# Optimization experiments

Hardware: AMD Instinct MI355X
Metric: run time of the kernel (lower is better)

Reference implementation:

```python
import math
import jax, jax.numpy as jnp
import numpy as np

B, T, E, H = 4, 2048, 1024, 16
D = E // H          # head_dim = 64
F = D // 2          # num_pairs = 32
FREQ_SIGMA = 1.0


def _build_spiral_frequencies(num_heads, num_pairs, freq_sigma):
    indices = np.arange(num_pairs, dtype=np.float32) + 0.5
    magnitudes = np.linspace(freq_sigma / max(num_pairs, 1), freq_sigma, num_pairs, dtype=np.float32)
    head_phases = np.linspace(0.0, 2.0 * math.pi, num_heads + 1, dtype=np.float32)[:-1][:, None]
    golden = (1.0 + math.sqrt(5.0)) / 2.0
    y = np.clip(1.0 - 2.0 * indices / float(num_pairs), -1.0, 1.0)
    radius = np.sqrt(np.clip(1.0 - y ** 2, 0.0, None))
    theta = (2.0 * math.pi * indices / golden)[None, :] + head_phases
    x = radius[None, :] * np.cos(theta)
    z = radius[None, :] * np.sin(theta)
    directions = np.stack([x, np.broadcast_to(y[None, :], (num_heads, num_pairs)), z], axis=-1)
    return (directions * magnitudes[None, :, None]).astype(np.float32)  # (H, F, 3)


def setup_inputs() -> dict:
    key = jax.random.key(0)
    ks = jax.random.split(key, 4)
    query = jax.random.normal(ks[0], (B, T, E), dtype=jnp.float32)
    positions = jax.random.normal(ks[1], (B, T, 3), dtype=jnp.float32)
    in_proj_weight = jax.random.normal(ks[2], (3 * E, E), dtype=jnp.float32) * (1.0 / math.sqrt(E))
    in_proj_bias = jnp.zeros((3 * E,), dtype=jnp.float32)
    out_proj_weight = jax.random.normal(ks[3], (E, E), dtype=jnp.float32) * (1.0 / math.sqrt(E))
    out_proj_bias = jnp.zeros((E,), dtype=jnp.float32)
    freqs = jnp.asarray(_build_spiral_frequencies(H, F, FREQ_SIGMA))
    return dict(query=query, positions=positions, in_proj_weight=in_proj_weight,
                in_proj_bias=in_proj_bias, out_proj_weight=out_proj_weight,
                out_proj_bias=out_proj_bias, freqs=freqs)


def _apply_rotary(x, positions, freqs):
    # x: (B, H, T, D), positions: (B, T, 3), freqs: (H, F, 3)
    angles = jnp.einsum('btd,hfd->bhtf', positions.astype(jnp.float32), freqs.astype(jnp.float32))
    cos = jnp.cos(angles).astype(x.dtype)
    sin = jnp.sin(angles).astype(x.dtype)
    xr = x.reshape(*x.shape[:-1], F, 2)
    x0, x1 = xr[..., 0], xr[..., 1]
    rotated = jnp.stack((x0 * cos - x1 * sin, x0 * sin + x1 * cos), axis=-1)
    return rotated.reshape(x.shape)  # rotary_dim == head_dim here


def reference(query, positions, in_proj_weight, in_proj_bias, out_proj_weight, out_proj_bias, freqs):
    b, t, e = query.shape
    h = freqs.shape[0]
    d = e // h
    # QKV projections (self-attention: all from query)
    q = query @ in_proj_weight[:e].T + in_proj_bias[:e]
    k = query @ in_proj_weight[e:2 * e].T + in_proj_bias[e:2 * e]
    v = query @ in_proj_weight[2 * e:].T + in_proj_bias[2 * e:]
    # split heads -> (B, H, T, D)
    q = q.reshape(b, t, h, d).transpose(0, 2, 1, 3)
    k = k.reshape(b, t, h, d).transpose(0, 2, 1, 3)
    v = v.reshape(b, t, h, d).transpose(0, 2, 1, 3)
    q = _apply_rotary(q, positions, freqs)
    k = _apply_rotary(k, positions, freqs)
    # SDPA
    scale = 1.0 / math.sqrt(d)
    scores = jnp.einsum('bhqd,bhkd->bhqk', q, k) * scale
    attn = jax.nn.softmax(scores, axis=-1)
    out = jnp.einsum('bhqk,bhkd->bhqd', attn, v)
    out = out.transpose(0, 2, 1, 3).reshape(b, t, e)
    return out @ out_proj_weight.T + out_proj_bias
```

## Files before the change

### kernel.cpp

```cpp
#include <hip/hip_runtime.h>
#include <math.h>

#define NB 4
#define NT 2048
#define NE 1024
#define NH 16
#define ND 64
#define NF 32

typedef _Float16 half8 __attribute__((ext_vector_type(8)));
typedef _Float16 half4 __attribute__((ext_vector_type(4)));
typedef unsigned int uint2v __attribute__((ext_vector_type(2)));
typedef unsigned int uint4v __attribute__((ext_vector_type(4)));
typedef float f32x4 __attribute__((ext_vector_type(4)));
typedef float f32x16 __attribute__((ext_vector_type(16)));
#define MFMA16(a, b, c) __builtin_amdgcn_mfma_f32_16x16x32_f16(a, b, c, 0, 0, 0)
#define MFMA32(a, b, c) __builtin_amdgcn_mfma_f32_32x32x16_f16(a, b, c, 0, 0, 0)

__device__ __forceinline__ float fast_exp2(float x) {
    float r;
    asm volatile("v_exp_f32 %0, %1" : "=v"(r) : "v"(x));
    return r;
}
__device__ __forceinline__ float max3f(float a, float b, float c) {
    return fmaxf(fmaxf(a, b), c);
}

__global__ __launch_bounds__(256)
void cvt_kernel(const float* __restrict__ X, const float* __restrict__ Wi,
                const float* __restrict__ Wo,
                _Float16* __restrict__ Xh, _Float16* __restrict__ Wih,
                _Float16* __restrict__ Woh)
{
    const size_t NX = (size_t)8388608, NWI = 3145728, NWO = 1048576;
    const size_t TOT = (NX + NWI + NWO) / 8;
    for (size_t gidx = (size_t)blockIdx.x*256 + threadIdx.x; gidx < TOT;
         gidx += (size_t)gridDim.x*256) {
        size_t i = gidx*8;
        const float* src; _Float16* dst; size_t off;
        if (i < NX)            { src = X;  dst = Xh;  off = i; }
        else if (i < NX + NWI) { src = Wi; dst = Wih; off = i - NX; }
        else                   { src = Wo; dst = Woh; off = i - NX - NWI; }
        float4 a = *(const float4*)(src + off);
        float4 b = *(const float4*)(src + off + 4);
        half8 h;
        h[0]=(_Float16)a.x; h[1]=(_Float16)a.y; h[2]=(_Float16)a.z; h[3]=(_Float16)a.w;
        h[4]=(_Float16)b.x; h[5]=(_Float16)b.y; h[6]=(_Float16)b.z; h[7]=(_Float16)b.w;
        *(half8*)(dst + off) = h;
    }
}

__global__ __launch_bounds__(256)
void qkv_mfma_kernel(const _Float16* __restrict__ Ah,
                     const _Float16* __restrict__ Bh,
                     const float* __restrict__ bias,
                     const float* __restrict__ pos,
                     const float* __restrict__ freqs,
                     _Float16* __restrict__ Qh,
                     _Float16* __restrict__ Kh,
                     _Float16* __restrict__ Vh)
{
    __shared__ _Float16 Ash[128*32];
    __shared__ _Float16 Bsh[128*32];

    const int tid = threadIdx.x;
    const int wid = tid >> 6, lane = tid & 63;
    const int ln = lane & 15, g = lane >> 4;
    const int wrow = wid >> 1, wcol = wid & 1;
    const int m0 = blockIdx.x * 128, n0 = blockIdx.y * 128;

    const int r0 = tid >> 2, s0 = tid & 3;
    const int k8 = s0 ^ ((r0 >> 1) & 3);
    const _Float16* gA0 = Ah + (size_t)(m0 + r0)      * NE + k8*8;
    const _Float16* gA1 = Ah + (size_t)(m0 + r0 + 64) * NE + k8*8;
    const _Float16* gB0 = Bh + (size_t)(n0 + r0)      * NE + k8*8;
    const _Float16* gB1 = Bh + (size_t)(n0 + r0 + 64) * NE + k8*8;

    const int xr = g ^ ((ln >> 1) & 3);

    f32x4 acc[4][4];
    #pragma unroll
    for (int i = 0; i < 4; ++i)
        #pragma unroll
        for (int j = 0; j < 4; ++j) acc[i][j] = (f32x4){0.f,0.f,0.f,0.f};

    half8 va0 = *(const half8*)gA0;
    half8 va1 = *(const half8*)gA1;
    half8 vb0 = *(const half8*)gB0;
    half8 vb1 = *(const half8*)gB1;

    for (int kt = 0; kt < NE; kt += 32) {
        if (kt) __syncthreads();
        *(half8*)&Ash[tid*8]       = va0;
        *(half8*)&Ash[(tid+256)*8] = va1;
        *(half8*)&Bsh[tid*8]       = vb0;
        *(half8*)&Bsh[(tid+256)*8] = vb1;
        __syncthreads();
        const int kn = kt + 32;
        if (kn < NE) {
            va0 = *(const half8*)(gA0 + kn);
            va1 = *(const half8*)(gA1 + kn);
            vb0 = *(const half8*)(gB0 + kn);
            vb1 = *(const half8*)(gB1 + kn);
        }
        half8 af[4], bf[4];
        #pragma unroll
        for (int mf = 0; mf < 4; ++mf)
            af[mf] = *(const half8*)&Ash[(wrow*64 + mf*16 + ln)*32 + xr*8];
        #pragma unroll
        for (int nf = 0; nf < 4; ++nf)
            bf[nf] = *(const half8*)&Bsh[(wcol*64 + nf*16 + ln)*32 + xr*8];
        __builtin_amdgcn_s_setprio(1);
        #pragma unroll
        for (int mf = 0; mf < 4; ++mf)
            #pragma unroll
            for (int nf = 0; nf < 4; ++nf)
                acc[mf][nf] = MFMA16(af[mf], bf[nf], acc[mf][nf]);
        __builtin_amdgcn_s_setprio(0);
    }

    const int sec = n0 >> 10;
    _Float16* dst = (sec == 0) ? Qh : (sec == 1) ? Kh : Vh;

    float cb[4], fx[4], fy[4], fz[4];
    int hh[4], dd[4];
    #pragma unroll
    for (int nf = 0; nf < 4; ++nf) {
        const int col = n0 + wcol*64 + nf*16 + ln;
        cb[nf] = bias[col];
        const int e = col & 1023;
        hh[nf] = e >> 6; dd[nf] = e & 63;
        if (sec != 2) {
            const float* fq = freqs + ((size_t)hh[nf]*NF + (dd[nf] >> 1))*3;
            fx[nf] = fq[0]; fy[nf] = fq[1]; fz[nf] = fq[2];
        }
    }
    const float sgn = (ln & 1) ? 1.0f : -1.0f;
    const float qs  = (sec == 0) ? 0.125f * 1.4426950408889634f : 1.0f;

    #pragma unroll
    for (int mf = 0; mf < 4; ++mf) {
        #pragma unroll
        for (int r = 0; r < 4; ++r) {
            const int m = m0 + wrow*64 + mf*16 + g*4 + r;
            const int b = m >> 11, t = m & 2047;
            if (sec == 2) {
                #pragma unroll
                for (int nf = 0; nf < 4; ++nf)
                    dst[((size_t)(b*NH + hh[nf])*NT + t)*ND + dd[nf]] =
                        (_Float16)(acc[mf][nf][r] + cb[nf]);
            } else {
                const float px = pos[(size_t)m*3 + 0];
                const float py = pos[(size_t)m*3 + 1];
                const float pz = pos[(size_t)m*3 + 2];
                #pragma unroll
                for (int nf = 0; nf < 4; ++nf) {
                    const float x  = acc[mf][nf][r] + cb[nf];
                    const float xo = __shfl_xor(x, 1);
                    const float ang = px*fx[nf] + py*fy[nf] + pz*fz[nf];
                    float sn, cs;
                    __sincosf(ang, &sn, &cs);
                    const float out = (x*cs + sgn*xo*sn) * qs;
                    dst[((size_t)(b*NH + hh[nf])*NT + t)*ND + dd[nf]] = (_Float16)out;
                }
            }
        }
    }
}

__global__ __launch_bounds__(256)
void attn_mfma_kernel(const _Float16* __restrict__ Qg, const _Float16* __restrict__ Kg,
                      const _Float16* __restrict__ Vg, _Float16* __restrict__ Og)
{
    __shared__ _Float16 Ks[2][64][68];
    __shared__ _Float16 VsT[2][64][68];

    const int tid  = threadIdx.x;
    const int wid  = tid >> 6;
    const int lane = tid & 63;
    const int m31  = lane & 31;
    const int hi   = lane >> 5;
    const int bh   = blockIdx.x;
    const int qt   = blockIdx.y;
    const int b = bh >> 4, h = bh & 15;
    const _Float16* Qp = Qg + (size_t)bh * NT * ND;
    const _Float16* Kp = Kg + (size_t)bh * NT * ND;
    const _Float16* Vp = Vg + (size_t)bh * NT * ND;

    const int qrow_g = qt*128 + wid*32 + m31;

    half8 qfr[4];
    #pragma unroll
    for (int c = 0; c < 4; ++c)
        qfr[c] = *(const half8*)(Qp + (size_t)qrow_g*ND + 16*c + 8*hi);

    f32x16 o0, o1;
    #pragma unroll
    for (int e = 0; e < 16; ++e) { o0[e] = 0.f; o1[e] = 0.f; }
    float m_i = 8.0f, l_i = 0.0f;

    const int sr  = tid >> 2;
    const int sc0 = (tid & 3) * 16;
    const int dp  = tid & 31;
    const int wv  = tid >> 5;
    const _Float16* kbase = Kp + (size_t)sr*ND + sc0;
    const _Float16* vbase = Vp + (size_t)(wv*8)*ND + 2*dp;

    half8 kv0, kv1;
    unsigned int vr[8];

    #define LOADREGS(off)  do {                                              \
        kv0 = *(const half8*)(kbase + (size_t)(off)*ND);                     \
        kv1 = *(const half8*)(kbase + (size_t)(off)*ND + 8);                 \
        _Pragma("unroll")                                                    \
        for (int j = 0; j < 8; ++j)                                          \
            vr[j] = *(const unsigned int*)(vbase + (size_t)((off) + j)*ND);  \
    } while (0)

    #define STOREBUF(bf)  do {                                               \
        *(half8*)&Ks[bf][sr][sc0]     = kv0;                                 \
        *(half8*)&Ks[bf][sr][sc0 + 8] = kv1;                                 \
        uint4v lod, hid;                                                     \
        _Pragma("unroll")                                                    \
        for (int j2 = 0; j2 < 4; ++j2) {                                     \
            lod[j2] = __builtin_amdgcn_perm(vr[2*j2+1], vr[2*j2], 0x05040100u); \
            hid[j2] = __builtin_amdgcn_perm(vr[2*j2+1], vr[2*j2], 0x07060302u); \
        }                                                                    \
        *(uint4v*)&VsT[bf][2*dp][wv*8]     = lod;                            \
        *(uint4v*)&VsT[bf][2*dp + 1][wv*8] = hid;                            \
    } while (0)

    LOADREGS(0);
    STOREBUF(0);
    LOADREGS(64);

    for (int t = 0; t < 32; ++t) {
        const int cur = t & 1;
        __syncthreads();
        if (t < 31) STOREBUF(cur ^ 1);
        if (t < 30) LOADREGS((t + 2) * 64);

        f32x16 st0, st1;
        const float mneg = -m_i;
        #pragma unroll
        for (int e = 0; e < 16; ++e) { st0[e] = mneg; st1[e] = mneg; }

        __builtin_amdgcn_s_setprio(1);
        #pragma unroll
        for (int c = 0; c < 4; ++c) {
            half8 kf0 = *(const half8*)&Ks[cur][m31][16*c + 8*hi];
            half8 kf1 = *(const half8*)&Ks[cur][32 + m31][16*c + 8*hi];
            st0 = MFMA32(kf0, qfr[c], st0);
            st1 = MFMA32(kf1, qfr[c], st1);
        }
        __builtin_amdgcn_s_setprio(0);

        float t0 = max3f(st0[0],  st0[1],  st0[2]);
        float t1 = max3f(st0[3],  st0[4],  st0[5]);
        float t2 = max3f(st0[6],  st0[7],  st0[8]);
        float t3 = max3f(st0[9],  st0[10], st0[11]);
        float t4 = max3f(st0[12], st0[13], st0[14]);
        float t5 = max3f(st0[15], st1[0],  st1[1]);
        float t6 = max3f(st1[2],  st1[3],  st1[4]);
        float t7 = max3f(st1[5],  st1[6],  st1[7]);
        float t8 = max3f(st1[8],  st1[9],  st1[10]);
        float t9 = max3f(st1[11], st1[12], st1[13]);
        float ta = fmaxf(st1[14], st1[15]);
        float u0 = max3f(t0, t1, t2);
        float u1 = max3f(t3, t4, t5);
        float u2 = max3f(t6, t7, t8);
        float u3 = fmaxf(t9, ta);
        float pmax = fmaxf(max3f(u0, u1, u2), u3);
        pmax = fmaxf(pmax, __shfl_xor(pmax, 32));

        if (!__all(pmax <= 8.0f)) {
            const float delta = (pmax > 8.0f) ? pmax : 0.0f;
            const float alpha = fast_exp2(-delta);
            m_i += delta;
            l_i *= alpha;
            #pragma unroll
            for (int reg = 0; reg < 16; ++reg) {
                const int qr = (reg & 3) + 8*(reg >> 2) + 4*hi;
                const float a = __shfl(alpha, qr);
                o0[reg] *= a; o1[reg] *= a;
            }
            #pragma unroll
            for (int e = 0; e < 16; ++e) { st0[e] -= delta; st1[e] -= delta; }
        }

        float r0 = 0.f, r1 = 0.f, r2 = 0.f, r3 = 0.f;
        unsigned int pku0[8], pku1[8];
        #pragma unroll
        for (int j = 0; j < 8; ++j) {
            const float pa0 = fast_exp2(st0[2*j]);
            const float pa1 = fast_exp2(st0[2*j + 1]);
            const float pb0 = fast_exp2(st1[2*j]);
            const float pb1 = fast_exp2(st1[2*j + 1]);
            if ((j & 1) == 0) { r0 += pa0 + pa1; r1 += pb0 + pb1; }
            else              { r2 += pa0 + pa1; r3 += pb0 + pb1; }
            pku0[j] = __builtin_bit_cast(unsigned int, __builtin_amdgcn_cvt_pkrtz(pa0, pa1));
            pku1[j] = __builtin_bit_cast(unsigned int, __builtin_amdgcn_cvt_pkrtz(pb0, pb1));
        }
        float rs = (r0 + r1) + (r2 + r3);
        rs += __shfl_xor(rs, 32);
        l_i += rs;

        #pragma unroll
        for (int kc = 0; kc < 4; ++kc) {
            const unsigned int a0 = (kc < 2) ? pku0[4*(kc & 1) + 0] : pku1[4*(kc & 1) + 0];
            const unsigned int a1 = (kc < 2) ? pku0[4*(kc & 1) + 1] : pku1[4*(kc & 1) + 1];
            const unsigned int b0 = (kc < 2) ? pku0[4*(kc & 1) + 2] : pku1[4*(kc & 1) + 2];
            const unsigned int b1 = (kc < 2) ? pku0[4*(kc & 1) + 3] : pku1[4*(kc & 1) + 3];
            uint2v rpa = __builtin_amdgcn_permlane32_swap(a0, b0, false, false);
            uint2v rpb = __builtin_amdgcn_permlane32_swap(a1, b1, false, false);
            uint4v u;
            u[0] = rpa[0]; u[1] = rpb[0]; u[2] = rpa[1]; u[3] = rpb[1];
            const half8 pa = __builtin_bit_cast(half8, u);
            const half8 vb0 = *(const half8*)&VsT[cur][m31][16*kc + 8*hi];
            const half8 vb1 = *(const half8*)&VsT[cur][32 + m31][16*kc + 8*hi];
            __builtin_amdgcn_s_setprio(1);
            o0 = MFMA32(pa, vb0, o0);
            o1 = MFMA32(pa, vb1, o1);
            __builtin_amdgcn_s_setprio(0);
        }
    }

    #pragma unroll
    for (int reg = 0; reg < 16; ++reg) {
        const int qr = (reg & 3) + 8*(reg >> 2) + 4*hi;
        const float lq  = __shfl(l_i, qr);
        const float inv = 1.0f / lq;
        const int qg = qt*128 + wid*32 + qr;
        _Float16* dstp = Og + ((size_t)b*NT + qg)*NE + h*ND;
        dstp[m31]      = (_Float16)(o0[reg] * inv);
        dstp[32 + m31] = (_Float16)(o1[reg] * inv);
    }
    #undef LOADREGS
    #undef STOREBUF
}

__global__ __launch_bounds__(256)
void out_proj_mfma_kernel(const _Float16* __restrict__ Ah,
                          const _Float16* __restrict__ Bh,
                          const float* __restrict__ bias,
                          float* __restrict__ out)
{
    __shared__ _Float16 Ash[128*32];
    __shared__ _Float16 Bsh[128*32];

    const int tid = threadIdx.x;
    const int wid = tid >> 6, lane = tid & 63;
    const int ln = lane & 15, g = lane >> 4;
    const int wrow = wid >> 1, wcol = wid & 1;
    const int m0 = blockIdx.x * 128, n0 = blockIdx.y * 128;

    const int r0 = tid >> 2, s0 = tid & 3;
    const int k8 = s0 ^ ((r0 >> 1) & 3);
    const _Float16* gA0 = Ah + (size_t)(m0 + r0)      * NE + k8*8;
    const _Float16* gA1 = Ah + (size_t)(m0 + r0 + 64) * NE + k8*8;
    const _Float16* gB0 = Bh + (size_t)(n0 + r0)      * NE + k8*8;
    const _Float16* gB1 = Bh + (size_t)(n0 + r0 + 64) * NE + k8*8;
    const int xr = g ^ ((ln >> 1) & 3);

    f32x4 acc[4][4];
    #pragma unroll
    for (int i = 0; i < 4; ++i)
        #pragma unroll
        for (int j = 0; j < 4; ++j) acc[i][j] = (f32x4){0.f,0.f,0.f,0.f};

    half8 va0 = *(const half8*)gA0;
    half8 va1 = *(const half8*)gA1;
    half8 vb0 = *(const half8*)gB0;
    half8 vb1 = *(const half8*)gB1;

    for (int kt = 0; kt < NE; kt += 32) {
        if (kt) __syncthreads();
        *(half8*)&Ash[tid*8]       = va0;
        *(half8*)&Ash[(tid+256)*8] = va1;
        *(half8*)&Bsh[tid*8]       = vb0;
        *(half8*)&Bsh[(tid+256)*8] = vb1;
        __syncthreads();
        const int kn = kt + 32;
        if (kn < NE) {
            va0 = *(const half8*)(gA0 + kn);
            va1 = *(const half8*)(gA1 + kn);
            vb0 = *(const half8*)(gB0 + kn);
            vb1 = *(const half8*)(gB1 + kn);
        }
        half8 af[4], bf[4];
        #pragma unroll
        for (int mf = 0; mf < 4; ++mf)
            af[mf] = *(const half8*)&Ash[(wrow*64 + mf*16 + ln)*32 + xr*8];
        #pragma unroll
        for (int nf = 0; nf < 4; ++nf)
            bf[nf] = *(const half8*)&Bsh[(wcol*64 + nf*16 + ln)*32 + xr*8];
        __builtin_amdgcn_s_setprio(1);
        #pragma unroll
        for (int mf = 0; mf < 4; ++mf)
            #pragma unroll
            for (int nf = 0; nf < 4; ++nf)
                acc[mf][nf] = MFMA16(af[mf], bf[nf], acc[mf][nf]);
        __builtin_amdgcn_s_setprio(0);
    }

    float cb[4];
    #pragma unroll
    for (int nf = 0; nf < 4; ++nf) cb[nf] = bias[n0 + wcol*64 + nf*16 + ln];

    #pragma unroll
    for (int mf = 0; mf < 4; ++mf)
        #pragma unroll
        for (int r = 0; r < 4; ++r) {
            const int m = m0 + wrow*64 + mf*16 + g*4 + r;
            #pragma unroll
            for (int nf = 0; nf < 4; ++nf)
                out[(size_t)m*NE + n0 + wcol*64 + nf*16 + ln] = acc[mf][nf][r] + cb[nf];
        }
}

extern "C" void kernel_launch(void* const* d_in, const int* in_sizes, int n_in,
                              void* d_out, int out_size, void* d_ws, size_t ws_size,
                              hipStream_t stream)
{
    const float* X   = (const float*)d_in[0];
    const float* pos = (const float*)d_in[1];
    const float* Wi  = (const float*)d_in[2];
    const float* bi  = (const float*)d_in[3];
    const float* Wo  = (const float*)d_in[4];
    const float* bo  = (const float*)d_in[5];
    const float* fr  = (const float*)d_in[6];
    float* out = (float*)d_out;

    _Float16* Xh  = (_Float16*)d_ws;
    _Float16* Wih = Xh  + 8388608;
    _Float16* Woh = Wih + 3145728;
    _Float16* Qh  = Woh + 1048576;
    _Float16* Kh  = Qh  + 8388608;
    _Float16* Vh  = Kh  + 8388608;
    _Float16* Oh  = Vh  + 8388608;

    cvt_kernel          <<<3072, 256, 0, stream>>>(X, Wi, Wo, Xh, Wih, Woh);
    qkv_mfma_kernel     <<<dim3(64, 24), 256, 0, stream>>>(Xh, Wih, bi, pos, fr, Qh, Kh, Vh);
    attn_mfma_kernel    <<<dim3(64, 16), 256, 0, stream>>>(Qh, Kh, Vh, Oh);
    out_proj_mfma_kernel<<<dim3(64, 8),  256, 0, stream>>>(Oh, Woh, bo, out);
}
```

Measured before the change: 242.5 us.

## Use 512-thread attention blocks and restructure softmax max tracking after exp

Each attention block now has 8 waves covering 256 query rows, so every staged K/V tile in shared memory serves twice as many queries, and the per-thread load share is halved. The softmax now exponentiates first and checks whether any probability exceeds 1, rescaling with log2/rcp only then. Row sums use packed fp16 dot products, and the PV MFMA loop runs under one priority raise. The trade-offs are lower fp16 precision in row sums and the rescaled probabilities, plus fewer blocks in the grid.

Measured after the change: 223.3 us. 7.9% less time.

```diff
diff --git a/kernel.cpp b/kernel.cpp
--- a/kernel.cpp
+++ b/kernel.cpp
@@ -9,7 +9,7 @@
 #define NF 32
 
 typedef _Float16 half8 __attribute__((ext_vector_type(8)));
-typedef _Float16 half4 __attribute__((ext_vector_type(4)));
+typedef __fp16 fp16x2 __attribute__((ext_vector_type(2)));
 typedef unsigned int uint2v __attribute__((ext_vector_type(2)));
 typedef unsigned int uint4v __attribute__((ext_vector_type(4)));
 typedef float f32x4 __attribute__((ext_vector_type(4)));
@@ -168,12 +168,12 @@
     }
 }
 
-__global__ __launch_bounds__(256)
+__global__ __launch_bounds__(512, 4)
 void attn_mfma_kernel(const _Float16* __restrict__ Qg, const _Float16* __restrict__ Kg,
                       const _Float16* __restrict__ Vg, _Float16* __restrict__ Og)
 {
-    __shared__ _Float16 Ks[2][64][68];
-    __shared__ _Float16 VsT[2][64][68];
+    __shared__ _Float16 Ks[2][64][70];
+    __shared__ _Float16 VsT[2][64][70];
 
     const int tid  = threadIdx.x;
     const int wid  = tid >> 6;
@@ -187,7 +187,7 @@
     const _Float16* Kp = Kg + (size_t)bh * NT * ND;
     const _Float16* Vp = Vg + (size_t)bh * NT * ND;
 
-    const int qrow_g = qt*128 + wid*32 + m31;
+    const int qrow_g = qt*256 + wid*32 + m31;
 
     half8 qfr[4];
     #pragma unroll
@@ -199,35 +199,32 @@
     for (int e = 0; e < 16; ++e) { o0[e] = 0.f; o1[e] = 0.f; }
     float m_i = 8.0f, l_i = 0.0f;
 
-    const int sr  = tid >> 2;
-    const int sc0 = (tid & 3) * 16;
+    const int sr  = tid >> 3;
+    const int sc0 = (tid & 7) * 8;
     const int dp  = tid & 31;
     const int wv  = tid >> 5;
     const _Float16* kbase = Kp + (size_t)sr*ND + sc0;
-    const _Float16* vbase = Vp + (size_t)(wv*8)*ND + 2*dp;
-
-    half8 kv0, kv1;
-    unsigned int vr[8];
+    const _Float16* vbase = Vp + (size_t)(wv*4)*ND + 2*dp;
+
+    half8 kv;
+    unsigned int vr[4];
 
     #define LOADREGS(off)  do {                                              \
-        kv0 = *(const half8*)(kbase + (size_t)(off)*ND);                     \
-        kv1 = *(const half8*)(kbase + (size_t)(off)*ND + 8);                 \
+        kv = *(const half8*)(kbase + (size_t)(off)*ND);                      \
         _Pragma("unroll")                                                    \
-        for (int j = 0; j < 8; ++j)                                          \
+        for (int j = 0; j < 4; ++j)                                          \
             vr[j] = *(const unsigned int*)(vbase + (size_t)((off) + j)*ND);  \
     } while (0)
 
     #define STOREBUF(bf)  do {                                               \
-        *(half8*)&Ks[bf][sr][sc0]     = kv0;                                 \
-        *(half8*)&Ks[bf][sr][sc0 + 8] = kv1;                                 \
-        uint4v lod, hid;                                                     \
-        _Pragma("unroll")                                                    \
-        for (int j2 = 0; j2 < 4; ++j2) {                                     \
-            lod[j2] = __builtin_amdgcn_perm(vr[2*j2+1], vr[2*j2], 0x05040100u); \
-            hid[j2] = __builtin_amdgcn_perm(vr[2*j2+1], vr[2*j2], 0x07060302u); \
-        }                                                                    \
-        *(uint4v*)&VsT[bf][2*dp][wv*8]     = lod;                            \
-        *(uint4v*)&VsT[bf][2*dp + 1][wv*8] = hid;                            \
+        *(half8*)&Ks[bf][sr][sc0] = kv;                                      \
+        uint2v lod, hid;                                                     \
+        lod[0] = __builtin_amdgcn_perm(vr[1], vr[0], 0x05040100u);           \
+        lod[1] = __builtin_amdgcn_perm(vr[3], vr[2], 0x05040100u);           \
+        hid[0] = __builtin_amdgcn_perm(vr[1], vr[0], 0x07060302u);           \
+        hid[1] = __builtin_amdgcn_perm(vr[3], vr[2], 0x07060302u);           \
+        *(uint2v*)&VsT[bf][2*dp][wv*4]     = lod;                            \
+        *(uint2v*)&VsT[bf][2*dp + 1][wv*4] = hid;                            \
     } while (0)
 
     LOADREGS(0);
@@ -255,56 +252,54 @@
         }
         __builtin_amdgcn_s_setprio(0);
 
-        float t0 = max3f(st0[0],  st0[1],  st0[2]);
-        float t1 = max3f(st0[3],  st0[4],  st0[5]);
-        float t2 = max3f(st0[6],  st0[7],  st0[8]);
-        float t3 = max3f(st0[9],  st0[10], st0[11]);
-        float t4 = max3f(st0[12], st0[13], st0[14]);
-        float t5 = max3f(st0[15], st1[0],  st1[1]);
-        float t6 = max3f(st1[2],  st1[3],  st1[4]);
-        float t7 = max3f(st1[5],  st1[6],  st1[7]);
-        float t8 = max3f(st1[8],  st1[9],  st1[10]);
-        float t9 = max3f(st1[11], st1[12], st1[13]);
-        float ta = fmaxf(st1[14], st1[15]);
-        float u0 = max3f(t0, t1, t2);
-        float u1 = max3f(t3, t4, t5);
-        float u2 = max3f(t6, t7, t8);
-        float u3 = fmaxf(t9, ta);
-        float pmax = fmaxf(max3f(u0, u1, u2), u3);
-        pmax = fmaxf(pmax, __shfl_xor(pmax, 32));
-
-        if (!__all(pmax <= 8.0f)) {
-            const float delta = (pmax > 8.0f) ? pmax : 0.0f;
-            const float alpha = fast_exp2(-delta);
+        const fp16x2 ones2 = {(__fp16)1.0f, (__fp16)1.0f};
+        unsigned int pku0[8], pku1[8];
+        float rsA = 0.f, rsB = 0.f;
+        float pmax = 0.f;
+        #pragma unroll
+        for (int j = 0; j < 8; ++j) {
+            const float pa0 = fast_exp2(st0[2*j]);
+            const float pa1 = fast_exp2(st0[2*j + 1]);
+            const float pb0 = fast_exp2(st1[2*j]);
+            const float pb1 = fast_exp2(st1[2*j + 1]);
+            const fp16x2 h2a = __builtin_amdgcn_cvt_pkrtz(pa0, pa1);
+            const fp16x2 h2b = __builtin_amdgcn_cvt_pkrtz(pb0, pb1);
+            pku0[j] = __builtin_bit_cast(unsigned int, h2a);
+            pku1[j] = __builtin_bit_cast(unsigned int, h2b);
+            rsA = __builtin_amdgcn_fdot2(h2a, ones2, rsA, false);
+            rsB = __builtin_amdgcn_fdot2(h2b, ones2, rsB, false);
+            pmax = max3f(pmax, pa0, pa1);
+            pmax = max3f(pmax, pb0, pb1);
+        }
+        float rs = rsA + rsB;
+        rs += __shfl_xor(rs, 32);
+
+        if (__any(pmax > 1.0f)) {
+            pmax = fmaxf(pmax, __shfl_xor(pmax, 32));
+            const bool  grow  = pmax > 1.0f;
+            const float delta = grow ? log2f(pmax) : 0.0f;
+            const float alpha = grow ? __builtin_amdgcn_rcpf(pmax) : 1.0f;
             m_i += delta;
             l_i *= alpha;
+            rs  *= alpha;
+            fp16x2 am; am[0] = (__fp16)alpha; am[1] = (__fp16)alpha;
+            #pragma unroll
+            for (int j = 0; j < 8; ++j) {
+                fp16x2 p0v = __builtin_bit_cast(fp16x2, pku0[j]) * am;
+                fp16x2 p1v = __builtin_bit_cast(fp16x2, pku1[j]) * am;
+                pku0[j] = __builtin_bit_cast(unsigned int, p0v);
+                pku1[j] = __builtin_bit_cast(unsigned int, p1v);
+            }
             #pragma unroll
             for (int reg = 0; reg < 16; ++reg) {
                 const int qr = (reg & 3) + 8*(reg >> 2) + 4*hi;
                 const float a = __shfl(alpha, qr);
                 o0[reg] *= a; o1[reg] *= a;
             }
-            #pragma unroll
-            for (int e = 0; e < 16; ++e) { st0[e] -= delta; st1[e] -= delta; }
-        }
-
-        float r0 = 0.f, r1 = 0.f, r2 = 0.f, r3 = 0.f;
-        unsigned int pku0[8], pku1[8];
-        #pragma unroll
-        for (int j = 0; j < 8; ++j) {
-            const float pa0 = fast_exp2(st0[2*j]);
-            const float pa1 = fast_exp2(st0[2*j + 1]);
-            const float pb0 = fast_exp2(st1[2*j]);
-            const float pb1 = fast_exp2(st1[2*j + 1]);
-            if ((j & 1) == 0) { r0 += pa0 + pa1; r1 += pb0 + pb1; }
-            else              { r2 += pa0 + pa1; r3 += pb0 + pb1; }
-            pku0[j] = __builtin_bit_cast(unsigned int, __builtin_amdgcn_cvt_pkrtz(pa0, pa1));
-            pku1[j] = __builtin_bit_cast(unsigned int, __builtin_amdgcn_cvt_pkrtz(pb0, pb1));
-        }
-        float rs = (r0 + r1) + (r2 + r3);
-        rs += __shfl_xor(rs, 32);
+        }
         l_i += rs;
 
+        __builtin_amdgcn_s_setprio(1);
         #pragma unroll
         for (int kc = 0; kc < 4; ++kc) {
             const unsigned int a0 = (kc < 2) ? pku0[4*(kc & 1) + 0] : pku1[4*(kc & 1) + 0];
@@ -318,11 +313,10 @@
             const half8 pa = __builtin_bit_cast(half8, u);
             const half8 vb0 = *(const half8*)&VsT[cur][m31][16*kc + 8*hi];
             const half8 vb1 = *(const half8*)&VsT[cur][32 + m31][16*kc + 8*hi];
-            __builtin_amdgcn_s_setprio(1);
             o0 = MFMA32(pa, vb0, o0);
             o1 = MFMA32(pa, vb1, o1);
-            __builtin_amdgcn_s_setprio(0);
-        }
+        }
+        __builtin_amdgcn_s_setprio(0);
     }
 
     #pragma unroll
@@ -330,7 +324,7 @@
         const int qr = (reg & 3) + 8*(reg >> 2) + 4*hi;
         const float lq  = __shfl(l_i, qr);
         const float inv = 1.0f / lq;
-        const int qg = qt*128 + wid*32 + qr;
+        const int qg = qt*256 + wid*32 + qr;
         _Float16* dstp = Og + ((size_t)b*NT + qg)*NE + h*ND;
         dstp[m31]      = (_Float16)(o0[reg] * inv);
         dstp[32 + m31] = (_Float16)(o1[reg] * inv);
@@ -441,6 +435,6 @@
 
     cvt_kernel          <<<3072, 256, 0, stream>>>(X, Wi, Wo, Xh, Wih, Woh);
     qkv_mfma_kernel     <<<dim3(64, 24), 256, 0, stream>>>(Xh, Wih, bi, pos, fr, Qh, Kh, Vh);
-    attn_mfma_kernel    <<<dim3(64, 16), 256, 0, stream>>>(Qh, Kh, Vh, Oh);
+    attn_mfma_kernel    <<<dim3(64, 8), 512, 0, stream>>>(Qh, Kh, Vh, Oh);
     out_proj_mfma_kernel<<<dim3(64, 8),  256, 0, stream>>>(Oh, Woh, bo, out);
 }
```
